# Performance work log

Hardware: AMD Instinct MI355X
Metric: run time of the kernel (lower is better)

## Reference

```python
import jax, jax.numpy as jnp
import numpy as np
from jax import lax

N, D, H, C = 4096, 1024, 512, 21  # rois, head feat dim, gcn hidden, n_classes


def setup_inputs() -> dict:
    key = jax.random.key(0)
    ks = jax.random.split(key, 9)
    x1 = jax.random.uniform(ks[0], (N,), minval=0.0, maxval=800.0)
    y1 = jax.random.uniform(ks[1], (N,), minval=0.0, maxval=800.0)
    w = jax.random.uniform(ks[2], (N,), minval=16.0, maxval=256.0)
    h = jax.random.uniform(ks[3], (N,), minval=16.0, maxval=256.0)
    rois = jnp.stack([x1, y1, x1 + w, y1 + h], axis=1)  # [N,4] x1,y1,x2,y2
    pooled_feat = jax.random.normal(ks[4], (N, D))
    Wg1 = jax.random.normal(ks[5], (D, H)) * 0.02
    bg1 = jnp.zeros((H,), jnp.float32)
    Wg2 = jax.random.normal(ks[6], (H, H)) * 0.02
    bg2 = jnp.zeros((H,), jnp.float32)
    W_bbox = jax.random.normal(ks[7], (H, 4 * C)) * 0.001
    b_bbox = jnp.zeros((4 * C,), jnp.float32)
    W_cls = jax.random.normal(ks[8], (H, C)) * 0.01
    b_cls = jnp.zeros((C,), jnp.float32)
    return dict(rois=rois, pooled_feat=pooled_feat, Wg1=Wg1, bg1=bg1, Wg2=Wg2,
                bg2=bg2, W_bbox=W_bbox, b_bbox=b_bbox, W_cls=W_cls, b_cls=b_cls)


def _iou_binary_adj(boxes):
    # bbox_overlaps_batch IoU (Pascal +1 convention), then binarize and zero diag
    x1, y1, x2, y2 = boxes[:, 0], boxes[:, 1], boxes[:, 2], boxes[:, 3]
    area = (x2 - x1 + 1.0) * (y2 - y1 + 1.0)
    iw = jnp.maximum(jnp.minimum(x2[:, None], x2[None, :]) - jnp.maximum(x1[:, None], x1[None, :]) + 1.0, 0.0)
    ih = jnp.maximum(jnp.minimum(y2[:, None], y2[None, :]) - jnp.maximum(y1[:, None], y1[None, :]) + 1.0, 0.0)
    inter = iw * ih
    iou = inter / (area[:, None] + area[None, :] - inter)
    adj = (iou > 0.0).astype(boxes.dtype)
    return adj * (1.0 - jnp.eye(boxes.shape[0], dtype=boxes.dtype))


def _connected_components(adj):
    # jit-friendly replacement for DFS subgraph_split: min-label propagation
    # with pointer jumping (converges in O(log diameter) iterations).
    n = adj.shape[0]
    labels0 = jnp.arange(n, dtype=jnp.int32)
    big = jnp.int32(n)

    def step(labels, _):
        nb = jnp.min(jnp.where(adj > 0.0, labels[None, :], big), axis=1)
        labels = jnp.minimum(labels, nb)
        labels = labels[labels]  # pointer jump
        return labels, None

    labels, _ = lax.scan(step, labels0, None, length=32)
    return labels  # component id per roi (min vertex index in component)


def _cosine_adj(x):
    # pairwise cosine similarity, diag zeroed (matches s != t loop)
    xn = x / jnp.maximum(jnp.linalg.norm(x, axis=1, keepdims=True), 1e-6)
    a = xn @ xn.T
    return a * (1.0 - jnp.eye(x.shape[0], dtype=x.dtype))


def reference(rois, pooled_feat, Wg1, bg1, Wg2, bg2, W_bbox, b_bbox, W_cls, b_cls):
    adj_bin = _iou_binary_adj(rois)          # [N,N] 0/1
    labels = _connected_components(adj_bin)  # [N] int32 subgraph ids
    A = _cosine_adj(pooled_feat)             # [N,N]
    h1 = jax.nn.relu(A @ (pooled_feat @ Wg1) + bg1)  # GCN layer 1
    h2 = jax.nn.relu(A @ (h1 @ Wg2) + bg2)           # GCN layer 2
    bbox_pred = h2 @ W_bbox + b_bbox          # [N, 4*C]
    cls_prob = jax.nn.softmax(h2 @ W_cls + b_cls, axis=1)  # [N, C]
    return labels, cls_prob, bbox_pred
```

## Files before the change

### kernel.cpp

```cpp
#include <hip/hip_runtime.h>
#include <hip/hip_bf16.h>
#include <stdint.h>


typedef __attribute__((ext_vector_type(8))) short short8;
typedef __attribute__((ext_vector_type(4))) float floatx4;

#define BK 32
#define LSTR 40

__device__ __forceinline__ unsigned short bfbits(float f) {
  union { float f; unsigned int i; } u; u.f = f;
  unsigned int r = u.i + 0x7fffu + ((u.i >> 16) & 1);
  return (unsigned short)(r >> 16);
}

template <int MODE>
__global__ __launch_bounds__(256) void gemm64(
    const __hip_bfloat16* __restrict__ P, const __hip_bfloat16* __restrict__ Q,
    int KC, int ld, int N, float* __restrict__ part,
    const float* __restrict__ rinorm, const __hip_bfloat16* __restrict__ ST,
    const float* __restrict__ bias, __hip_bfloat16* __restrict__ outb) {
  __shared__ short As[2][64 * LSTR];
  __shared__ short Bs[2][64 * LSTR];
  const int tid = threadIdx.x;
  const int w = tid >> 6, lane = tid & 63;
  const size_t m0 = (size_t)blockIdx.y * 64, n0 = (size_t)blockIdx.x * 64;
  const int z = blockIdx.z;

  const int srow = tid >> 2, skoff = (tid & 3) * 8;
  const short* gA = (const short*)P + (m0 + srow) * (size_t)ld + (size_t)z * KC + skoff;
  const short* gB = (const short*)Q + (n0 + srow) * (size_t)ld + (size_t)z * KC + skoff;
  const int soff = srow * LSTR + skoff;

  const int wm = (w >> 1) * 32, wn = (w & 1) * 32;
  const int lr = lane & 15, ko = (lane >> 4) * 8;

  floatx4 acc[2][2];
#pragma unroll
  for (int i = 0; i < 2; ++i)
#pragma unroll
    for (int j = 0; j < 2; ++j) acc[i][j] = (floatx4){0.f, 0.f, 0.f, 0.f};

  const int nIter = KC / BK;
  short8 ra = *(const short8*)gA;
  short8 rb = *(const short8*)gB;
  *(short8*)&As[0][soff] = ra;
  *(short8*)&Bs[0][soff] = rb;
  if (nIter > 1) {
    ra = *(const short8*)(gA + BK);
    rb = *(const short8*)(gB + BK);
  }
  __syncthreads();

  for (int it = 0; it < nIter; ++it) {
    const int cur = it & 1;
    short8 av[2], bv[2];
#pragma unroll
    for (int t = 0; t < 2; ++t) av[t] = *(const short8*)&As[cur][(wm + t * 16 + lr) * LSTR + ko];
#pragma unroll
    for (int t = 0; t < 2; ++t) bv[t] = *(const short8*)&Bs[cur][(wn + t * 16 + lr) * LSTR + ko];
    if (it + 1 < nIter) {
      *(short8*)&As[cur ^ 1][soff] = ra;
      *(short8*)&Bs[cur ^ 1][soff] = rb;
      if (it + 2 < nIter) {
        const int off = (it + 2) * BK;
        ra = *(const short8*)(gA + off);
        rb = *(const short8*)(gB + off);
      }
    }
#pragma unroll
    for (int i = 0; i < 2; ++i)
#pragma unroll
      for (int j = 0; j < 2; ++j)
        acc[i][j] = __builtin_amdgcn_mfma_f32_16x16x32_bf16(av[i], bv[j], acc[i][j], 0, 0, 0);
    __syncthreads();
  }

  const size_t MN = (size_t)(gridDim.y * 64) * (size_t)N;
  float* cp = part + (size_t)z * MN;
  const int rb4 = (lane >> 4) * 4;
#pragma unroll
  for (int i = 0; i < 2; ++i)
#pragma unroll
    for (int j = 0; j < 2; ++j)
#pragma unroll
      for (int r = 0; r < 4; ++r) {
        int row = (int)m0 + wm + i * 16 + rb4 + r;
        int col = (int)n0 + wn + j * 16 + lr;
        float v = acc[i][j][r];
        if (MODE == 0) {
          cp[(size_t)row * N + col] = v;
        } else if (MODE == 1) {
          outb[(size_t)row * 4096 + col] = __float2bfloat16(v);
        } else {
          v = rinorm[row] * v - __bfloat162float(ST[(size_t)col * 4096 + row]) + bias[col];
          outb[(size_t)row * 512 + col] = __float2bfloat16(fmaxf(v, 0.f));
        }
      }
}

__global__ void k_red0(const float* __restrict__ part, __hip_bfloat16* __restrict__ out, int n) {
  int i = (blockIdx.x * 256 + threadIdx.x) * 4;
  if (i >= n) return;
  float4 v = *(const float4*)(part + i);
  for (int s = 1; s < 8; ++s) {
    float4 q = *(const float4*)(part + (size_t)s * n + i);
    v.x += q.x; v.y += q.y; v.z += q.z; v.w += q.w;
  }
  out[i] = __float2bfloat16(v.x);
  out[i + 1] = __float2bfloat16(v.y);
  out[i + 2] = __float2bfloat16(v.z);
  out[i + 3] = __float2bfloat16(v.w);
}

__global__ void k_red2soft(const float* __restrict__ part, const float* __restrict__ bb,
                           const float* __restrict__ bc, float* __restrict__ bbox,
                           float* __restrict__ cls) {
  const size_t MN = 4096ull * 128;
  int row = (blockIdx.x * 256 + threadIdx.x) >> 6;
  int lane = threadIdx.x & 63;
  size_t b = (size_t)row * 128 + lane;
  float v0 = part[b] + part[MN + b] + part[2 * MN + b] + part[3 * MN + b];
  float v1 = part[b + 64] + part[MN + b + 64] + part[2 * MN + b + 64] + part[3 * MN + b + 64];
  bbox[(size_t)row * 84 + lane] = v0 + bb[lane];
  if (lane < 20) bbox[(size_t)row * 84 + 64 + lane] = v1 + bb[64 + lane];
  float lsrc = (lane >= 20 && lane < 41) ? v1 + bc[lane - 20] : 0.f;
  float lj = __shfl(lsrc, 20 + lane);
  float x = (lane < 21) ? lj : -1e30f;
  float m = x;
  for (int o = 16; o; o >>= 1) m = fmaxf(m, __shfl_xor(m, o));
  float e = (lane < 21) ? expf(x - m) : 0.f;
  float s = e;
  for (int o = 16; o; o >>= 1) s += __shfl_xor(s, o);
  if (lane < 21) cls[(size_t)row * 21 + lane] = e / s;
}

__global__ void k_nf(const float* __restrict__ X, __hip_bfloat16* __restrict__ Xb,
                     float* __restrict__ rinorm) {
  int wave = (blockIdx.x * 256 + threadIdx.x) >> 6;
  int lane = threadIdx.x & 63;
  const float4* row = (const float4*)(X + (size_t)wave * 1024);
  uint2* orow = (uint2*)((short*)Xb + (size_t)wave * 1024);
  float s = 0.f;
#pragma unroll
  for (int it = 0; it < 4; ++it) {
    float4 p = row[lane + it * 64];
    s += p.x * p.x + p.y * p.y + p.z * p.z + p.w * p.w;
    uint2 q;
    q.x = (unsigned int)bfbits(p.x) | ((unsigned int)bfbits(p.y) << 16);
    q.y = (unsigned int)bfbits(p.z) | ((unsigned int)bfbits(p.w) << 16);
    orow[lane + it * 64] = q;
  }
  for (int o = 32; o; o >>= 1) s += __shfl_down(s, o);
  if (lane == 0) rinorm[wave] = 1.f / fmaxf(sqrtf(s), 1e-6f);
}

__global__ void k_prep(const __hip_bfloat16* __restrict__ Xb, const float* __restrict__ rinorm,
                       const float* __restrict__ Wg1, const float* __restrict__ Wg2,
                       const float* __restrict__ Wb, const float* __restrict__ Wc,
                       __hip_bfloat16* __restrict__ XRT, __hip_bfloat16* __restrict__ Wg1T,
                       __hip_bfloat16* __restrict__ Wg2T, __hip_bfloat16* __restrict__ WcatT) {
  __shared__ float s[32][33];
  const int tid = threadIdx.x;
  const int tx = tid & 31, ty = tid >> 5;
  int blk = blockIdx.x;
  if (blk < 4096) {
    int c0 = (blk & 31) * 32, r0 = (blk >> 5) * 32;
#pragma unroll
    for (int k = 0; k < 4; ++k) {
      int r = r0 + ty + k * 8;
      s[ty + k * 8][tx] = __bfloat162float(Xb[(size_t)r * 1024 + c0 + tx]) * rinorm[r];
    }
    __syncthreads();
#pragma unroll
    for (int k = 0; k < 4; ++k)
      XRT[(size_t)(c0 + ty + k * 8) * 4096 + r0 + tx] = __float2bfloat16(s[tx][ty + k * 8]);
  } else if (blk < 4608) {
    int l = blk - 4096;
    int c0 = (l & 15) * 32, r0 = (l >> 4) * 32;
#pragma unroll
    for (int k = 0; k < 4; ++k)
      s[ty + k * 8][tx] = Wg1[(size_t)(r0 + ty + k * 8) * 512 + c0 + tx];
    __syncthreads();
#pragma unroll
    for (int k = 0; k < 4; ++k)
      Wg1T[(size_t)(c0 + ty + k * 8) * 1024 + r0 + tx] = __float2bfloat16(s[tx][ty + k * 8]);
  } else if (blk < 4864) {
    int l = blk - 4608;
    int c0 = (l & 15) * 32, r0 = (l >> 4) * 32;
#pragma unroll
    for (int k = 0; k < 4; ++k)
      s[ty + k * 8][tx] = Wg2[(size_t)(r0 + ty + k * 8) * 512 + c0 + tx];
    __syncthreads();
#pragma unroll
    for (int k = 0; k < 4; ++k)
      Wg2T[(size_t)(c0 + ty + k * 8) * 512 + r0 + tx] = __float2bfloat16(s[tx][ty + k * 8]);
  } else {
    int idx = (blk - 4864) * 256 + tid;
    int r = idx >> 9, k = idx & 511;
    float v = 0.f;
    if (r < 84) v = Wb[(size_t)k * 84 + r];
    else if (r < 105) v = Wc[(size_t)k * 21 + (r - 84)];
    WcatT[idx] = __float2bfloat16(v);
  }
}

__global__ void k_adj(const float4* __restrict__ rois, unsigned long long* __restrict__ adj,
                      int* __restrict__ labels) {
  int wave = (blockIdx.x * 256 + threadIdx.x) >> 6;
  int lane = threadIdx.x & 63;
  float4 bi = rois[wave];
  unsigned long long myword = 0;
  int mn = wave;
  for (int w = 0; w < 64; ++w) {
    int j = w * 64 + lane;
    float4 bj = rois[j];
    float iw = fminf(bi.z, bj.z) - fmaxf(bi.x, bj.x) + 1.0f;
    float ih = fminf(bi.w, bj.w) - fmaxf(bi.y, bj.y) + 1.0f;
    bool ov = (iw > 0.f) && (ih > 0.f) && (j != wave);
    unsigned long long msk = __ballot(ov);
    if (lane == w) myword = msk;
    if (msk) mn = min(mn, w * 64 + (int)__builtin_ctzll(msk));
  }
  adj[(size_t)wave * 64 + lane] = myword;
  if (lane == 0) labels[wave] = mn;
}

__global__ void k_minprop(const unsigned long long* __restrict__ adj, int* __restrict__ labels) {
  int wave = (blockIdx.x * 256 + threadIdx.x) >> 6;
  int lane = threadIdx.x & 63;
  unsigned long long w = adj[(size_t)wave * 64 + lane];
  int m = 0x7fffffff;
  while (w) {
    int b = __builtin_ctzll(w);
    w &= w - 1;
    m = min(m, labels[lane * 64 + b]);
  }
  for (int o = 32; o; o >>= 1) m = min(m, __shfl_down(m, o));
  if (lane == 0 && m < labels[wave]) atomicMin(&labels[wave], m);
}

__global__ void k_jump(int* __restrict__ labels, float* __restrict__ outL) {
  __shared__ int a[4096];
  __shared__ int b[4096];
  int t = threadIdx.x;
  for (int i = t; i < 4096; i += 1024) a[i] = labels[i];
  __syncthreads();
  int* src = a;
  int* dst = b;
  for (int it = 0; it < 12; ++it) {
    for (int i = t; i < 4096; i += 1024) dst[i] = src[src[i]];
    __syncthreads();
    int* tp = src; src = dst; dst = tp;
  }
  for (int i = t; i < 4096; i += 1024) outL[i] = (float)src[i];
}

extern "C" void kernel_launch(void* const* d_in, const int* in_sizes, int n_in,
                              void* d_out, int out_size, void* d_ws, size_t ws_size,
                              hipStream_t stream) {
  const float* rois = (const float*)d_in[0];
  const float* X    = (const float*)d_in[1];
  const float* Wg1  = (const float*)d_in[2];
  const float* bg1  = (const float*)d_in[3];
  const float* Wg2  = (const float*)d_in[4];
  const float* bg2  = (const float*)d_in[5];
  const float* Wb   = (const float*)d_in[6];
  const float* bb   = (const float*)d_in[7];
  const float* Wc   = (const float*)d_in[8];
  const float* bc   = (const float*)d_in[9];

  float* out        = (float*)d_out;
  float* out_labels = out;
  float* out_cls    = out + 4096;
  float* out_bbox   = out + 4096 + 4096 * 21;

  char* p = (char*)d_ws;
  auto carve = [&](size_t bytes) { char* r = p; p += (bytes + 255) & ~(size_t)255; return r; };
  int* labels           = (int*)carve(4096ull * 4);
  float* rinorm         = (float*)carve(4096ull * 4);
  __hip_bfloat16* WcatT = (__hip_bfloat16*)carve(128ull * 512 * 2);
  __hip_bfloat16* Wg2T  = (__hip_bfloat16*)carve(512ull * 512 * 2);
  __hip_bfloat16* Wg1T  = (__hip_bfloat16*)carve(512ull * 1024 * 2);
  __hip_bfloat16* T2T   = (__hip_bfloat16*)carve(512ull * 1024 * 2);
  __hip_bfloat16* h     = (__hip_bfloat16*)carve(4096ull * 512 * 2);
  __hip_bfloat16* ST    = (__hip_bfloat16*)carve(512ull * 4096 * 2);
  __hip_bfloat16* Xb    = (__hip_bfloat16*)carve(4096ull * 1024 * 2);
  __hip_bfloat16* XRT   = (__hip_bfloat16*)carve(1024ull * 4096 * 2);
  unsigned long long* adj = (unsigned long long*)carve(4096ull * 64 * 8);
  float* part           = (float*)carve(16ull * 1024 * 1024);

  k_nf<<<1024, 256, 0, stream>>>(X, Xb, rinorm);
  k_prep<<<5120, 256, 0, stream>>>(Xb, rinorm, Wg1, Wg2, Wb, Wc, XRT, Wg1T, Wg2T, WcatT);

  k_adj<<<1024, 256, 0, stream>>>((const float4*)rois, adj, labels);
  for (int r = 0; r < 5; ++r) k_minprop<<<1024, 256, 0, stream>>>(adj, labels);
  k_jump<<<1, 1024, 0, stream>>>(labels, out_labels);

  gemm64<1><<<dim3(64, 8), 256, 0, stream>>>(Wg1T, Xb, 1024, 1024, 4096, part,
                                             nullptr, nullptr, nullptr, ST);
  gemm64<0><<<dim3(16, 8, 8), 256, 0, stream>>>(ST, XRT, 512, 4096, 1024, part,
                                                nullptr, nullptr, nullptr, nullptr);
  k_red0<<<512, 256, 0, stream>>>(part, T2T, 512 * 1024);
  gemm64<2><<<dim3(8, 64), 256, 0, stream>>>(Xb, T2T, 1024, 1024, 512, part,
                                             rinorm, ST, bg1, h);
  gemm64<1><<<dim3(64, 8), 256, 0, stream>>>(Wg2T, h, 512, 512, 4096, part,
                                             nullptr, nullptr, nullptr, ST);
  gemm64<0><<<dim3(16, 8, 8), 256, 0, stream>>>(ST, XRT, 512, 4096, 1024, part,
                                                nullptr, nullptr, nullptr, nullptr);
  k_red0<<<512, 256, 0, stream>>>(part, T2T, 512 * 1024);
  gemm64<2><<<dim3(8, 64), 256, 0, stream>>>(Xb, T2T, 1024, 1024, 512, part,
                                             rinorm, ST, bg2, h);
  gemm64<0><<<dim3(2, 64, 4), 256, 0, stream>>>(h, WcatT, 128, 512, 128, part,
                                                nullptr, nullptr, nullptr, nullptr);
  k_red2soft<<<1024, 256, 0, stream>>>(part, bb, bc, out_bbox, out_cls);
}
```

Before: 237.3 us.

## Fuse connected-components stages into GEMM and prep launches to cut kernel count

Folds the IoU adjacency build into the normalization kernel, runs the three min-propagation passes as extra blocks inside the prep and first two GEMM launches, and merges pointer jumping into the first reduction kernel. The final head GEMM drops split-K and reads a single partial directly. This removes many small serial launches and lets label propagation run alongside independent work. Min-propagation now runs three passes instead of five, with concurrent atomicMin updates inside each launch, so label convergence relies on the asynchronous propagation plus 12 pointer jumps.

```diff
diff --git a/kernel.cpp b/kernel.cpp
--- a/kernel.cpp
+++ b/kernel.cpp
@@ -16,21 +16,21 @@
 }
 
 template <int MODE>
-__global__ __launch_bounds__(256) void gemm64(
+__device__ __forceinline__ void dev_gemm(
     const __hip_bfloat16* __restrict__ P, const __hip_bfloat16* __restrict__ Q,
     int KC, int ld, int N, float* __restrict__ part,
     const float* __restrict__ rinorm, const __hip_bfloat16* __restrict__ ST,
-    const float* __restrict__ bias, __hip_bfloat16* __restrict__ outb) {
+    const float* __restrict__ bias, __hip_bfloat16* __restrict__ outb,
+    int bx, int by, int bz, int gy) {
   __shared__ short As[2][64 * LSTR];
   __shared__ short Bs[2][64 * LSTR];
   const int tid = threadIdx.x;
   const int w = tid >> 6, lane = tid & 63;
-  const size_t m0 = (size_t)blockIdx.y * 64, n0 = (size_t)blockIdx.x * 64;
-  const int z = blockIdx.z;
+  const size_t m0 = (size_t)by * 64, n0 = (size_t)bx * 64;
 
   const int srow = tid >> 2, skoff = (tid & 3) * 8;
-  const short* gA = (const short*)P + (m0 + srow) * (size_t)ld + (size_t)z * KC + skoff;
-  const short* gB = (const short*)Q + (n0 + srow) * (size_t)ld + (size_t)z * KC + skoff;
+  const short* gA = (const short*)P + (m0 + srow) * (size_t)ld + (size_t)bz * KC + skoff;
+  const short* gB = (const short*)Q + (n0 + srow) * (size_t)ld + (size_t)bz * KC + skoff;
   const int soff = srow * LSTR + skoff;
 
   const int wm = (w >> 1) * 32, wn = (w & 1) * 32;
@@ -77,8 +77,8 @@
     __syncthreads();
   }
 
-  const size_t MN = (size_t)(gridDim.y * 64) * (size_t)N;
-  float* cp = part + (size_t)z * MN;
+  const size_t MN = (size_t)(gy * 64) * (size_t)N;
+  float* cp = part + (size_t)bz * MN;
   const int rb4 = (lane >> 4) * 4;
 #pragma unroll
   for (int i = 0; i < 2; ++i)
@@ -100,9 +100,21 @@
       }
 }
 
-__global__ void k_red0(const float* __restrict__ part, __hip_bfloat16* __restrict__ out, int n) {
-  int i = (blockIdx.x * 256 + threadIdx.x) * 4;
-  if (i >= n) return;
+__device__ __forceinline__ void dev_minprop(const unsigned long long* __restrict__ adj,
+                                            int* __restrict__ labels, int node, int lane) {
+  unsigned long long w = adj[(size_t)node * 64 + lane];
+  int m = 0x7fffffff;
+  while (w) {
+    int b = __builtin_ctzll(w);
+    w &= w - 1;
+    m = min(m, labels[lane * 64 + b]);
+  }
+  for (int o = 32; o; o >>= 1) m = min(m, __shfl_down(m, o));
+  if (lane == 0 && m < labels[node]) atomicMin(&labels[node], m);
+}
+
+__device__ __forceinline__ void dev_red0(const float* __restrict__ part,
+                                         __hip_bfloat16* __restrict__ out, int n, int i) {
   float4 v = *(const float4*)(part + i);
   for (int s = 1; s < 8; ++s) {
     float4 q = *(const float4*)(part + (size_t)s * n + i);
@@ -114,15 +126,167 @@
   out[i + 3] = __float2bfloat16(v.w);
 }
 
-__global__ void k_red2soft(const float* __restrict__ part, const float* __restrict__ bb,
-                           const float* __restrict__ bc, float* __restrict__ bbox,
-                           float* __restrict__ cls) {
-  const size_t MN = 4096ull * 128;
+__global__ __launch_bounds__(256) void K_nf_adj(
+    const float* __restrict__ X, __hip_bfloat16* __restrict__ Xb, float* __restrict__ rinorm,
+    const float4* __restrict__ rois, unsigned long long* __restrict__ adj,
+    int* __restrict__ labels) {
+  int blk = blockIdx.x, tid = threadIdx.x;
+  int lane = tid & 63;
+  if (blk < 1024) {
+    int wave = (blk * 256 + tid) >> 6;
+    const float4* row = (const float4*)(X + (size_t)wave * 1024);
+    uint2* orow = (uint2*)((short*)Xb + (size_t)wave * 1024);
+    float s = 0.f;
+#pragma unroll
+    for (int it = 0; it < 4; ++it) {
+      float4 p = row[lane + it * 64];
+      s += p.x * p.x + p.y * p.y + p.z * p.z + p.w * p.w;
+      uint2 q;
+      q.x = (unsigned int)bfbits(p.x) | ((unsigned int)bfbits(p.y) << 16);
+      q.y = (unsigned int)bfbits(p.z) | ((unsigned int)bfbits(p.w) << 16);
+      orow[lane + it * 64] = q;
+    }
+    for (int o = 32; o; o >>= 1) s += __shfl_down(s, o);
+    if (lane == 0) rinorm[wave] = 1.f / fmaxf(sqrtf(s), 1e-6f);
+  } else {
+    int node = ((blk - 1024) * 256 + tid) >> 6;
+    float4 bi = rois[node];
+    unsigned long long myword = 0;
+    int mn = node;
+    for (int w = 0; w < 64; ++w) {
+      int j = w * 64 + lane;
+      float4 bj = rois[j];
+      float iw = fminf(bi.z, bj.z) - fmaxf(bi.x, bj.x) + 1.0f;
+      float ih = fminf(bi.w, bj.w) - fmaxf(bi.y, bj.y) + 1.0f;
+      bool ov = (iw > 0.f) && (ih > 0.f) && (j != node);
+      unsigned long long msk = __ballot(ov);
+      if (lane == w) myword = msk;
+      if (msk) mn = min(mn, w * 64 + (int)__builtin_ctzll(msk));
+    }
+    adj[(size_t)node * 64 + lane] = myword;
+    if (lane == 0) labels[node] = mn;
+  }
+}
+
+__global__ __launch_bounds__(256) void K_prep_mp(
+    const __hip_bfloat16* __restrict__ Xb, const float* __restrict__ rinorm,
+    const float* __restrict__ Wg1, const float* __restrict__ Wg2,
+    const float* __restrict__ Wb, const float* __restrict__ Wc,
+    __hip_bfloat16* __restrict__ XRT, __hip_bfloat16* __restrict__ Wg1T,
+    __hip_bfloat16* __restrict__ Wg2T, __hip_bfloat16* __restrict__ WcatT,
+    const unsigned long long* __restrict__ adj, int* __restrict__ labels) {
+  __shared__ float s[32][33];
+  const int tid = threadIdx.x;
+  const int tx = tid & 31, ty = tid >> 5;
+  int blk = blockIdx.x;
+  if (blk < 4096) {
+    int c0 = (blk & 31) * 32, r0 = (blk >> 5) * 32;
+#pragma unroll
+    for (int k = 0; k < 4; ++k) {
+      int r = r0 + ty + k * 8;
+      s[ty + k * 8][tx] = __bfloat162float(Xb[(size_t)r * 1024 + c0 + tx]) * rinorm[r];
+    }
+    __syncthreads();
+#pragma unroll
+    for (int k = 0; k < 4; ++k)
+      XRT[(size_t)(c0 + ty + k * 8) * 4096 + r0 + tx] = __float2bfloat16(s[tx][ty + k * 8]);
+  } else if (blk < 4608) {
+    int l = blk - 4096;
+    int c0 = (l & 15) * 32, r0 = (l >> 4) * 32;
+#pragma unroll
+    for (int k = 0; k < 4; ++k)
+      s[ty + k * 8][tx] = Wg1[(size_t)(r0 + ty + k * 8) * 512 + c0 + tx];
+    __syncthreads();
+#pragma unroll
+    for (int k = 0; k < 4; ++k)
+      Wg1T[(size_t)(c0 + ty + k * 8) * 1024 + r0 + tx] = __float2bfloat16(s[tx][ty + k * 8]);
+  } else if (blk < 4864) {
+    int l = blk - 4608;
+    int c0 = (l & 15) * 32, r0 = (l >> 4) * 32;
+#pragma unroll
+    for (int k = 0; k < 4; ++k)
+      s[ty + k * 8][tx] = Wg2[(size_t)(r0 + ty + k * 8) * 512 + c0 + tx];
+    __syncthreads();
+#pragma unroll
+    for (int k = 0; k < 4; ++k)
+      Wg2T[(size_t)(c0 + ty + k * 8) * 512 + r0 + tx] = __float2bfloat16(s[tx][ty + k * 8]);
+  } else if (blk < 5120) {
+    int idx = (blk - 4864) * 256 + tid;
+    int r = idx >> 9, k = idx & 511;
+    float v = 0.f;
+    if (r < 84) v = Wb[(size_t)k * 84 + r];
+    else if (r < 105) v = Wc[(size_t)k * 21 + (r - 84)];
+    WcatT[idx] = __float2bfloat16(v);
+  } else {
+    int node = ((blk - 5120) * 256 + tid) >> 6;
+    dev_minprop(adj, labels, node, tid & 63);
+  }
+}
+
+template <int MODE>
+__global__ __launch_bounds__(256) void K_gemm_mp(
+    const __hip_bfloat16* __restrict__ P, const __hip_bfloat16* __restrict__ Q,
+    int KC, int ld, int N, float* __restrict__ part,
+    const float* __restrict__ rinorm, const __hip_bfloat16* __restrict__ ST,
+    const float* __restrict__ bias, __hip_bfloat16* __restrict__ outb,
+    int gx, int gy, int gemmBlocks,
+    const unsigned long long* __restrict__ adj, int* __restrict__ labels) {
+  int blk = blockIdx.x;
+  if (blk < gemmBlocks) {
+    int bx = blk % gx, by = (blk / gx) % gy, bz = blk / (gx * gy);
+    dev_gemm<MODE>(P, Q, KC, ld, N, part, rinorm, ST, bias, outb, bx, by, bz, gy);
+  } else {
+    int node = ((blk - gemmBlocks) * 256 + threadIdx.x) >> 6;
+    dev_minprop(adj, labels, node, threadIdx.x & 63);
+  }
+}
+
+template <int MODE>
+__global__ __launch_bounds__(256) void K_gemm(
+    const __hip_bfloat16* __restrict__ P, const __hip_bfloat16* __restrict__ Q,
+    int KC, int ld, int N, float* __restrict__ part,
+    const float* __restrict__ rinorm, const __hip_bfloat16* __restrict__ ST,
+    const float* __restrict__ bias, __hip_bfloat16* __restrict__ outb, int gx, int gy) {
+  int blk = blockIdx.x;
+  int bx = blk % gx, by = (blk / gx) % gy, bz = blk / (gx * gy);
+  dev_gemm<MODE>(P, Q, KC, ld, N, part, rinorm, ST, bias, outb, bx, by, bz, gy);
+}
+
+__global__ __launch_bounds__(256) void K_red0_jump(
+    const float* __restrict__ part, __hip_bfloat16* __restrict__ out, int n,
+    int* __restrict__ labels, float* __restrict__ outL) {
+  int blk = blockIdx.x, t = threadIdx.x;
+  if (blk < 512) {
+    dev_red0(part, out, n, (blk * 256 + t) * 4);
+  } else {
+    __shared__ int a[4096];
+    __shared__ int b[4096];
+    for (int i = t; i < 4096; i += 256) a[i] = labels[i];
+    __syncthreads();
+    int* src = a;
+    int* dst = b;
+    for (int it = 0; it < 12; ++it) {
+      for (int i = t; i < 4096; i += 256) dst[i] = src[src[i]];
+      __syncthreads();
+      int* tp = src; src = dst; dst = tp;
+    }
+    for (int i = t; i < 4096; i += 256) outL[i] = (float)src[i];
+  }
+}
+
+__global__ __launch_bounds__(256) void K_red0(const float* __restrict__ part,
+                                              __hip_bfloat16* __restrict__ out, int n) {
+  dev_red0(part, out, n, (blockIdx.x * 256 + threadIdx.x) * 4);
+}
+
+__global__ __launch_bounds__(256) void K_red2soft(
+    const float* __restrict__ part, const float* __restrict__ bb, const float* __restrict__ bc,
+    float* __restrict__ bbox, float* __restrict__ cls) {
   int row = (blockIdx.x * 256 + threadIdx.x) >> 6;
   int lane = threadIdx.x & 63;
   size_t b = (size_t)row * 128 + lane;
-  float v0 = part[b] + part[MN + b] + part[2 * MN + b] + part[3 * MN + b];
-  float v1 = part[b + 64] + part[MN + b + 64] + part[2 * MN + b + 64] + part[3 * MN + b + 64];
+  float v0 = part[b];
+  float v1 = part[b + 64];
   bbox[(size_t)row * 84 + lane] = v0 + bb[lane];
   if (lane < 20) bbox[(size_t)row * 84 + 64 + lane] = v1 + bb[64 + lane];
   float lsrc = (lane >= 20 && lane < 41) ? v1 + bc[lane - 20] : 0.f;
@@ -134,127 +298,6 @@
   float s = e;
   for (int o = 16; o; o >>= 1) s += __shfl_xor(s, o);
   if (lane < 21) cls[(size_t)row * 21 + lane] = e / s;
-}
-
-__global__ void k_nf(const float* __restrict__ X, __hip_bfloat16* __restrict__ Xb,
-                     float* __restrict__ rinorm) {
-  int wave = (blockIdx.x * 256 + threadIdx.x) >> 6;
-  int lane = threadIdx.x & 63;
-  const float4* row = (const float4*)(X + (size_t)wave * 1024);
-  uint2* orow = (uint2*)((short*)Xb + (size_t)wave * 1024);
-  float s = 0.f;
-#pragma unroll
-  for (int it = 0; it < 4; ++it) {
-    float4 p = row[lane + it * 64];
-    s += p.x * p.x + p.y * p.y + p.z * p.z + p.w * p.w;
-    uint2 q;
-    q.x = (unsigned int)bfbits(p.x) | ((unsigned int)bfbits(p.y) << 16);
-    q.y = (unsigned int)bfbits(p.z) | ((unsigned int)bfbits(p.w) << 16);
-    orow[lane + it * 64] = q;
-  }
-  for (int o = 32; o; o >>= 1) s += __shfl_down(s, o);
-  if (lane == 0) rinorm[wave] = 1.f / fmaxf(sqrtf(s), 1e-6f);
-}
-
-__global__ void k_prep(const __hip_bfloat16* __restrict__ Xb, const float* __restrict__ rinorm,
-                       const float* __restrict__ Wg1, const float* __restrict__ Wg2,
-                       const float* __restrict__ Wb, const float* __restrict__ Wc,
-                       __hip_bfloat16* __restrict__ XRT, __hip_bfloat16* __restrict__ Wg1T,
-                       __hip_bfloat16* __restrict__ Wg2T, __hip_bfloat16* __restrict__ WcatT) {
-  __shared__ float s[32][33];
-  const int tid = threadIdx.x;
-  const int tx = tid & 31, ty = tid >> 5;
-  int blk = blockIdx.x;
-  if (blk < 4096) {
-    int c0 = (blk & 31) * 32, r0 = (blk >> 5) * 32;
-#pragma unroll
-    for (int k = 0; k < 4; ++k) {
-      int r = r0 + ty + k * 8;
-      s[ty + k * 8][tx] = __bfloat162float(Xb[(size_t)r * 1024 + c0 + tx]) * rinorm[r];
-    }
-    __syncthreads();
-#pragma unroll
-    for (int k = 0; k < 4; ++k)
-      XRT[(size_t)(c0 + ty + k * 8) * 4096 + r0 + tx] = __float2bfloat16(s[tx][ty + k * 8]);
-  } else if (blk < 4608) {
-    int l = blk - 4096;
-    int c0 = (l & 15) * 32, r0 = (l >> 4) * 32;
-#pragma unroll
-    for (int k = 0; k < 4; ++k)
-      s[ty + k * 8][tx] = Wg1[(size_t)(r0 + ty + k * 8) * 512 + c0 + tx];
-    __syncthreads();
-#pragma unroll
-    for (int k = 0; k < 4; ++k)
-      Wg1T[(size_t)(c0 + ty + k * 8) * 1024 + r0 + tx] = __float2bfloat16(s[tx][ty + k * 8]);
-  } else if (blk < 4864) {
-    int l = blk - 4608;
-    int c0 = (l & 15) * 32, r0 = (l >> 4) * 32;
-#pragma unroll
-    for (int k = 0; k < 4; ++k)
-      s[ty + k * 8][tx] = Wg2[(size_t)(r0 + ty + k * 8) * 512 + c0 + tx];
-    __syncthreads();
-#pragma unroll
-    for (int k = 0; k < 4; ++k)
-      Wg2T[(size_t)(c0 + ty + k * 8) * 512 + r0 + tx] = __float2bfloat16(s[tx][ty + k * 8]);
-  } else {
-    int idx = (blk - 4864) * 256 + tid;
-    int r = idx >> 9, k = idx & 511;
-    float v = 0.f;
-    if (r < 84) v = Wb[(size_t)k * 84 + r];
-    else if (r < 105) v = Wc[(size_t)k * 21 + (r - 84)];
-    WcatT[idx] = __float2bfloat16(v);
-  }
-}
-
-__global__ void k_adj(const float4* __restrict__ rois, unsigned long long* __restrict__ adj,
-                      int* __restrict__ labels) {
-  int wave = (blockIdx.x * 256 + threadIdx.x) >> 6;
-  int lane = threadIdx.x & 63;
-  float4 bi = rois[wave];
-  unsigned long long myword = 0;
-  int mn = wave;
-  for (int w = 0; w < 64; ++w) {
-    int j = w * 64 + lane;
-    float4 bj = rois[j];
-    float iw = fminf(bi.z, bj.z) - fmaxf(bi.x, bj.x) + 1.0f;
-    float ih = fminf(bi.w, bj.w) - fmaxf(bi.y, bj.y) + 1.0f;
-    bool ov = (iw > 0.f) && (ih > 0.f) && (j != wave);
-    unsigned long long msk = __ballot(ov);
-    if (lane == w) myword = msk;
-    if (msk) mn = min(mn, w * 64 + (int)__builtin_ctzll(msk));
-  }
-  adj[(size_t)wave * 64 + lane] = myword;
-  if (lane == 0) labels[wave] = mn;
-}
-
-__global__ void k_minprop(const unsigned long long* __restrict__ adj, int* __restrict__ labels) {
-  int wave = (blockIdx.x * 256 + threadIdx.x) >> 6;
-  int lane = threadIdx.x & 63;
-  unsigned long long w = adj[(size_t)wave * 64 + lane];
-  int m = 0x7fffffff;
-  while (w) {
-    int b = __builtin_ctzll(w);
-    w &= w - 1;
-    m = min(m, labels[lane * 64 + b]);
-  }
-  for (int o = 32; o; o >>= 1) m = min(m, __shfl_down(m, o));
-  if (lane == 0 && m < labels[wave]) atomicMin(&labels[wave], m);
-}
-
-__global__ void k_jump(int* __restrict__ labels, float* __restrict__ outL) {
-  __shared__ int a[4096];
-  __shared__ int b[4096];
-  int t = threadIdx.x;
-  for (int i = t; i < 4096; i += 1024) a[i] = labels[i];
-  __syncthreads();
-  int* src = a;
-  int* dst = b;
-  for (int it = 0; it < 12; ++it) {
-    for (int i = t; i < 4096; i += 1024) dst[i] = src[src[i]];
-    __syncthreads();
-    int* tp = src; src = dst; dst = tp;
-  }
-  for (int i = t; i < 4096; i += 1024) outL[i] = (float)src[i];
 }
 
 extern "C" void kernel_launch(void* const* d_in, const int* in_sizes, int n_in,
@@ -291,28 +334,26 @@
   unsigned long long* adj = (unsigned long long*)carve(4096ull * 64 * 8);
   float* part           = (float*)carve(16ull * 1024 * 1024);
 
-  k_nf<<<1024, 256, 0, stream>>>(X, Xb, rinorm);
-  k_prep<<<5120, 256, 0, stream>>>(Xb, rinorm, Wg1, Wg2, Wb, Wc, XRT, Wg1T, Wg2T, WcatT);
-
-  k_adj<<<1024, 256, 0, stream>>>((const float4*)rois, adj, labels);
-  for (int r = 0; r < 5; ++r) k_minprop<<<1024, 256, 0, stream>>>(adj, labels);
-  k_jump<<<1, 1024, 0, stream>>>(labels, out_labels);
-
-  gemm64<1><<<dim3(64, 8), 256, 0, stream>>>(Wg1T, Xb, 1024, 1024, 4096, part,
-                                             nullptr, nullptr, nullptr, ST);
-  gemm64<0><<<dim3(16, 8, 8), 256, 0, stream>>>(ST, XRT, 512, 4096, 1024, part,
-                                                nullptr, nullptr, nullptr, nullptr);
-  k_red0<<<512, 256, 0, stream>>>(part, T2T, 512 * 1024);
-  gemm64<2><<<dim3(8, 64), 256, 0, stream>>>(Xb, T2T, 1024, 1024, 512, part,
-                                             rinorm, ST, bg1, h);
-  gemm64<1><<<dim3(64, 8), 256, 0, stream>>>(Wg2T, h, 512, 512, 4096, part,
-                                             nullptr, nullptr, nullptr, ST);
-  gemm64<0><<<dim3(16, 8, 8), 256, 0, stream>>>(ST, XRT, 512, 4096, 1024, part,
-                                                nullptr, nullptr, nullptr, nullptr);
-  k_red0<<<512, 256, 0, stream>>>(part, T2T, 512 * 1024);
-  gemm64<2><<<dim3(8, 64), 256, 0, stream>>>(Xb, T2T, 1024, 1024, 512, part,
-                                             rinorm, ST, bg2, h);
-  gemm64<0><<<dim3(2, 64, 4), 256, 0, stream>>>(h, WcatT, 128, 512, 128, part,
-                                                nullptr, nullptr, nullptr, nullptr);
-  k_red2soft<<<1024, 256, 0, stream>>>(part, bb, bc, out_bbox, out_cls);
-}
+  K_nf_adj<<<2048, 256, 0, stream>>>(X, Xb, rinorm, (const float4*)rois, adj, labels);
+  K_prep_mp<<<6144, 256, 0, stream>>>(Xb, rinorm, Wg1, Wg2, Wb, Wc,
+                                      XRT, Wg1T, Wg2T, WcatT, adj, labels);
+  K_gemm_mp<1><<<512 + 1024, 256, 0, stream>>>(Wg1T, Xb, 1024, 1024, 4096, part,
+                                               nullptr, nullptr, nullptr, ST,
+                                               64, 8, 512, adj, labels);
+  K_gemm_mp<0><<<1024 + 1024, 256, 0, stream>>>(ST, XRT, 512, 4096, 1024, part,
+                                                nullptr, nullptr, nullptr, nullptr,
+                                                16, 8, 1024, adj, labels);
+  K_red0_jump<<<513, 256, 0, stream>>>(part, T2T, 512 * 1024, labels, out_labels);
+  K_gemm<2><<<512, 256, 0, stream>>>(Xb, T2T, 1024, 1024, 512, part,
+                                     rinorm, ST, bg1, h, 8, 64);
+  K_gemm<1><<<512, 256, 0, stream>>>(Wg2T, h, 512, 512, 4096, part,
+                                     nullptr, nullptr, nullptr, ST, 64, 8);
+  K_gemm<0><<<1024, 256, 0, stream>>>(ST, XRT, 512, 4096, 1024, part,
+                                      nullptr, nullptr, nullptr, nullptr, 16, 8);
+  K_red0<<<512, 256, 0, stream>>>(part, T2T, 512 * 1024);
+  K_gemm<2><<<512, 256, 0, stream>>>(Xb, T2T, 1024, 1024, 512, part,
+                                     rinorm, ST, bg2, h, 8, 64);
+  K_gemm<0><<<128, 256, 0, stream>>>(h, WcatT, 512, 512, 128, part,
+                                     nullptr, nullptr, nullptr, nullptr, 2, 64);
+  K_red2soft<<<1024, 256, 0, stream>>>(part, bb, bc, out_bbox, out_cls);
+}
```

After: 247.0 us. 4.1% more time.
